# Performance work log

Measured on AMD Instinct MI355X. Metric: run time of the kernel, lower is better.

## Reference

```python
import jax, jax.numpy as jnp
import numpy as np

V_FEATS = 1024; N1 = 800; N2 = 800; K = 10
CONV = [256, 128]; DENSE = [256, 64]


def setup_inputs() -> dict:
    key = jax.random.key(0)
    ks = jax.random.split(key, 20)
    inp = {
        "Z1": jax.random.normal(ks[0], (N1, V_FEATS), jnp.float32),
        "nb1": jax.random.randint(ks[2], (N1, K), -1, N1),
        "Z2": jax.random.normal(ks[1], (N2, V_FEATS), jnp.float32),
        "nb2": jax.random.randint(ks[3], (N2, K), -1, N2),
    }
    j = 4
    dims = [V_FEATS] + CONV
    for i, (di, do) in enumerate(zip(dims[:-1], dims[1:])):
        s = 1.0 / np.sqrt(di)
        inp[f"Wr{i}"] = jax.random.normal(ks[j], (di, do), jnp.float32) * s; j += 1
        inp[f"Wnr{i}"] = jax.random.normal(ks[j], (di, do), jnp.float32) * s; j += 1
    fdims = [2 * CONV[-1]] + DENSE + [1]
    for i, (di, do) in enumerate(zip(fdims[:-1], fdims[1:])):
        s = 1.0 / np.sqrt(di)
        inp[f"fW{i}"] = jax.random.normal(ks[j], (di, do), jnp.float32) * s; j += 1
        inp[f"fb{i}"] = jnp.zeros((do,), jnp.float32)
    return inp


def gnn_layer(Z, nb, Wr, Wnr):
    # residue (self) signal and neighbor base signal
    res = Z @ Wr                                  # [N, F]
    base = Z @ Wnr                                # [N, F]
    mask = nb > -1                                # [N, K]
    feats = base[nb] * mask[..., None]            # gather (neg idx wrap, masked out)
    norm = jnp.maximum(mask.sum(1), 1).astype(Z.dtype)  # [N], avoid div-by-0
    return jax.nn.relu(res + feats.sum(1) / norm[:, None])


def _forward(Z1, nb1, Z2, nb2, Wr0, Wnr0, Wr1, Wnr1, fW0, fb0, fW1, fb1, fW2, fb2):
    # two stacked GNN layers per protein (shared weights across the two proteins)
    x1 = gnn_layer(gnn_layer(Z1, nb1, Wr0, Wnr0), nb1, Wr1, Wnr1)  # [N1, F]
    x2 = gnn_layer(gnn_layer(Z2, nb2, Wr0, Wnr0), nb2, Wr1, Wnr1)  # [N2, F]
    n1, F = x1.shape
    n2 = x2.shape[0]
    # all-pairs concat: itertools.product(rows(x1), rows(x2)) -> [N1*N2, 2F]
    pairs = jnp.concatenate(
        [jnp.broadcast_to(x1[:, None, :], (n1, n2, F)),
         jnp.broadcast_to(x2[None, :, :], (n1, n2, F))], axis=-1
    ).reshape(n1 * n2, 2 * F)
    h = jax.nn.relu(pairs @ fW0 + fb0)
    h = jax.nn.relu(h @ fW1 + fb1)
    return jnp.squeeze(h @ fW2 + fb2)             # [N1*N2]


def reference(Z1, nb1, Z2, nb2, Wr0, Wnr0, Wr1, Wnr1, fW0, fb0, fW1, fb1, fW2, fb2):
    return _forward(Z1, nb1, Z2, nb2, Wr0, Wnr0, Wr1, Wnr1,
                    fW0, fb0, fW1, fb1, fW2, fb2)
```

## Files before the change

kernel.cpp:

```cpp
#include <hip/hip_runtime.h>
#include <hip/hip_bf16.h>
#include <cstdint>
#include <cstddef>


typedef __bf16 bf16_t;
typedef __bf16 bf16x4 __attribute__((ext_vector_type(4)));
typedef __bf16 bf16x8 __attribute__((ext_vector_type(8)));
typedef float f32x4 __attribute__((ext_vector_type(4)));
typedef _Float16 f16_t;
typedef _Float16 f16x8 __attribute__((ext_vector_type(8)));

static __device__ __forceinline__ f32x4 mfma_bf16(bf16x8 a, bf16x8 b, f32x4 c) {
  return __builtin_amdgcn_mfma_f32_16x16x32_bf16(a, b, c, 0, 0, 0);
}
static __device__ __forceinline__ f32x4 mfma_f16(f16x8 a, f16x8 b, f32x4 c) {
  return __builtin_amdgcn_mfma_f32_16x16x32_f16(a, b, c, 0, 0, 0);
}

#define N1R 800
#define NR  1600
#define VF  1024
#define F0  256
#define F1  128

static __device__ __forceinline__ void split8(float4 va, float4 vb,
                                              bf16x8& h8, bf16x8& l8) {
  float v[8] = {va.x, va.y, va.z, va.w, vb.x, vb.y, vb.z, vb.w};
  #pragma unroll
  for (int e = 0; e < 8; ++e) {
    bf16_t h = (bf16_t)v[e];
    h8[e] = h;
    l8[e] = (bf16_t)(v[e] - (float)h);
  }
}

__global__ void conv_agg(const float* __restrict__ Z1, const float* __restrict__ Z2,
                         const int* __restrict__ nb1, const int* __restrict__ nb2,
                         const float* __restrict__ Wr0, const float* __restrict__ Wnr0,
                         const float* __restrict__ Wr1, const float* __restrict__ Wnr1,
                         const float* __restrict__ fW0, const float* __restrict__ fW1,
                         const float* __restrict__ fb1, const float* __restrict__ fW2,
                         const float* __restrict__ fb2,
                         bf16_t* __restrict__ W0h, bf16_t* __restrict__ W0l,
                         bf16_t* __restrict__ W1h, bf16_t* __restrict__ W1l,
                         bf16_t* __restrict__ fAh, bf16_t* __restrict__ fAl,
                         bf16_t* __restrict__ fBh, bf16_t* __restrict__ fBl,
                         f16_t* __restrict__ fW1th, float* __restrict__ fbw,
                         bf16_t* __restrict__ Zah, bf16_t* __restrict__ Zal) {
  int wb = blockIdx.x;
  int tid = threadIdx.x;
  if (wb >= 2625) {
    int r = wb - 2625;
    const int* nbp;
    const float* Zp;
    if (r < N1R) { nbp = nb1 + r * 10; Zp = Z1; }
    else         { nbp = nb2 + (r - N1R) * 10; Zp = Z2; }
    int c4 = tid * 4;
    float4 s = make_float4(0.f, 0.f, 0.f, 0.f);
    int cnt = 0;
    #pragma unroll
    for (int k = 0; k < 10; ++k) {
      int idx = nbp[k];
      if (idx > -1) {
        cnt++;
        float4 v = *(const float4*)(Zp + (size_t)idx * VF + c4);
        s.x += v.x; s.y += v.y; s.z += v.z; s.w += v.w;
      }
    }
    float inv = 1.f / (float)(cnt > 0 ? cnt : 1);
    float vv[4] = {s.x * inv, s.y * inv, s.z * inv, s.w * inv};
    bf16x4 h4, l4;
    #pragma unroll
    for (int e = 0; e < 4; ++e) {
      bf16_t h = (bf16_t)vv[e];
      h4[e] = h;
      l4[e] = (bf16_t)(vv[e] - (float)h);
    }
    *(bf16x4*)(Zah + (size_t)r * VF + c4) = h4;
    *(bf16x4*)(Zal + (size_t)r * VF + c4) = l4;
    return;
  }
  if (wb >= 2560 && wb < 2624) {
    int t = (wb - 2560) * 256 + tid;
    int n = t & 63;
    int k = t >> 6;
    fW1th[(n << 8) + k] = (f16_t)fW1[k * 64 + n];
    return;
  }
  if (wb == 2624) {
    if (tid < 128) {
      int jl = tid & 15, s = tid >> 4;
      fbw[jl * 8 + s] = (s < 4) ? fb1[s * 16 + jl] : fW2[(s - 4) * 16 + jl];
    } else if (tid == 128) {
      fbw[128] = fb2[0];
    }
    return;
  }
  const float* src; bf16_t* dh; bf16_t* dl; int ld, lk, ln, b0;
  if      (wb < 1024) { src = Wr0;  ld = 256; lk = 10; ln = 8; dh = W0h;              dl = W0l;              b0 = 0;    }
  else if (wb < 2048) { src = Wnr0; ld = 256; lk = 10; ln = 8; dh = W0h + 256 * 1024; dl = W0l + 256 * 1024; b0 = 1024; }
  else if (wb < 2176) { src = Wr1;  ld = 128; lk = 8;  ln = 7; dh = W1h;              dl = W1l;              b0 = 2048; }
  else if (wb < 2304) { src = Wnr1; ld = 128; lk = 8;  ln = 7; dh = W1h + 128 * 256;  dl = W1l + 128 * 256;  b0 = 2176; }
  else if (wb < 2432) { src = fW0;             ld = 256; lk = 7; ln = 8; dh = fAh;    dl = fAl;              b0 = 2304; }
  else                { src = fW0 + 128 * 256; ld = 256; lk = 7; ln = 8; dh = fBh;    dl = fBl;              b0 = 2432; }
  int t = (wb - b0) * 256 + tid;
  int n = t & ((1 << ln) - 1);
  int k = t >> ln;
  float v = src[k * ld + n];
  bf16_t h = (bf16_t)v;
  dh[(n << lk) + k] = h;
  dl[(n << lk) + k] = (bf16_t)(v - (float)h);
}

__global__ __launch_bounds__(256) void gemm_l1(
    const float* __restrict__ Z1, const float* __restrict__ Z2,
    const bf16_t* __restrict__ Zah, const bf16_t* __restrict__ Zal,
    const bf16_t* __restrict__ W0h, const bf16_t* __restrict__ W0l,
    float* __restrict__ P) {
  int lane = threadIdx.x & 63;
  int w = threadIdx.x >> 6;
  int jl = lane & 15, hi = lane >> 4;

  int row0 = blockIdx.y * 16;
  int col = blockIdx.x * 64 + w * 16 + jl;
  int z = blockIdx.z;
  int half = z >> 1;
  int kStart = (z & 1) * 512;
  int r = row0 + jl;

  const size_t WOFF = (size_t)half * 256 * 1024;
  const bf16_t* pBh = W0h + WOFF + (size_t)col * 1024 + hi * 8 + kStart;
  const bf16_t* pBl = W0l + WOFF + (size_t)col * 1024 + hi * 8 + kStart;

  f32x4 accE = {}, accO = {};
  if (half == 0) {
    const float* pZ = ((r < N1R) ? Z1 + (size_t)r * VF
                                 : Z2 + (size_t)(r - N1R) * VF) + hi * 8 + kStart;
    for (int kb = 0; kb < 512; kb += 128) {
      float4 za[4][2];
      bf16x8 bh[4], bl[4];
      #pragma unroll
      for (int u = 0; u < 4; ++u) {
        za[u][0] = *(const float4*)(pZ + kb + u * 32);
        za[u][1] = *(const float4*)(pZ + kb + u * 32 + 4);
        bh[u] = *(const bf16x8*)(pBh + kb + u * 32);
        bl[u] = *(const bf16x8*)(pBl + kb + u * 32);
      }
      #pragma unroll
      for (int u = 0; u < 4; ++u) {
        bf16x8 ah, al;
        split8(za[u][0], za[u][1], ah, al);
        f32x4& acc = (u & 1) ? accO : accE;
        acc = mfma_bf16(ah, bh[u], acc);
        acc = mfma_bf16(al, bh[u], acc);
        acc = mfma_bf16(ah, bl[u], acc);
      }
    }
  } else {
    const bf16_t* pAh = Zah + (size_t)r * VF + hi * 8 + kStart;
    const bf16_t* pAl = Zal + (size_t)r * VF + hi * 8 + kStart;
    for (int kb = 0; kb < 512; kb += 128) {
      bf16x8 ah[4], al[4], bh[4], bl[4];
      #pragma unroll
      for (int u = 0; u < 4; ++u) {
        ah[u] = *(const bf16x8*)(pAh + kb + u * 32);
        al[u] = *(const bf16x8*)(pAl + kb + u * 32);
        bh[u] = *(const bf16x8*)(pBh + kb + u * 32);
        bl[u] = *(const bf16x8*)(pBl + kb + u * 32);
      }
      #pragma unroll
      for (int u = 0; u < 4; ++u) {
        f32x4& acc = (u & 1) ? accO : accE;
        acc = mfma_bf16(ah[u], bh[u], acc);
        acc = mfma_bf16(al[u], bh[u], acc);
        acc = mfma_bf16(ah[u], bl[u], acc);
      }
    }
  }
  float* Pz = P + (size_t)z * NR * F0;
  #pragma unroll
  for (int reg = 0; reg < 4; ++reg) {
    int row = row0 + hi * 4 + reg;
    Pz[(size_t)row * F0 + col] = accE[reg] + accO[reg];
  }
}

__global__ void agg1_kernel(const float* __restrict__ P,
                            const int* __restrict__ nb1, const int* __restrict__ nb2,
                            bf16_t* __restrict__ H0h, bf16_t* __restrict__ H0l,
                            bf16_t* __restrict__ Gah, bf16_t* __restrict__ Gal) {
  int r = blockIdx.x;
  int c = threadIdx.x;
  const size_t PS = (size_t)NR * F0;
  const int* nbp;
  int roff;
  if (r < N1R) { nbp = nb1 + r * 10; roff = 0; }
  else         { nbp = nb2 + (r - N1R) * 10; roff = N1R; }
  size_t so = (size_t)r * F0 + c;
  float v = fmaxf(P[so] + P[so + PS] + P[so + 2 * PS] + P[so + 3 * PS], 0.f);
  bf16_t h = (bf16_t)v;
  H0h[so] = h;
  H0l[so] = (bf16_t)(v - (float)h);
  float s = 0.f; int cnt = 0;
  #pragma unroll
  for (int k = 0; k < 10; ++k) {
    int idx = nbp[k];
    if (idx > -1) {
      cnt++;
      size_t o = (size_t)(roff + idx) * F0 + c;
      s += fmaxf(P[o] + P[o + PS] + P[o + 2 * PS] + P[o + 3 * PS], 0.f);
    }
  }
  float g = s / (float)(cnt > 0 ? cnt : 1);
  bf16_t gh = (bf16_t)g;
  Gah[so] = gh;
  Gal[so] = (bf16_t)(g - (float)gh);
}

__global__ __launch_bounds__(256) void gemm_l2(
    const bf16_t* __restrict__ H0h, const bf16_t* __restrict__ H0l,
    const bf16_t* __restrict__ Gah, const bf16_t* __restrict__ Gal,
    const bf16_t* __restrict__ W1h, const bf16_t* __restrict__ W1l,
    float* __restrict__ P2) {
  int lane = threadIdx.x & 63;
  int w = threadIdx.x >> 6;
  int jl = lane & 15, hi = lane >> 4;

  int row0 = blockIdx.y * 16;
  int col = blockIdx.x * 64 + w * 16 + jl;
  int z = blockIdx.z;
  int r = row0 + jl;

  const bf16_t* pAh = (z ? Gah : H0h) + (size_t)r * F0 + hi * 8;
  const bf16_t* pAl = (z ? Gal : H0l) + (size_t)r * F0 + hi * 8;
  const size_t WOFF = (size_t)z * 128 * 256;
  const bf16_t* pBh = W1h + WOFF + (size_t)col * 256 + hi * 8;
  const bf16_t* pBl = W1l + WOFF + (size_t)col * 256 + hi * 8;

  f32x4 accE = {}, accO = {};
  for (int kb = 0; kb < 256; kb += 128) {
    bf16x8 ah[4], al[4], bh[4], bl[4];
    #pragma unroll
    for (int u = 0; u < 4; ++u) {
      ah[u] = *(const bf16x8*)(pAh + kb + u * 32);
      al[u] = *(const bf16x8*)(pAl + kb + u * 32);
      bh[u] = *(const bf16x8*)(pBh + kb + u * 32);
      bl[u] = *(const bf16x8*)(pBl + kb + u * 32);
    }
    #pragma unroll
    for (int u = 0; u < 4; ++u) {
      f32x4& acc = (u & 1) ? accO : accE;
      acc = mfma_bf16(ah[u], bh[u], acc);
      acc = mfma_bf16(al[u], bh[u], acc);
      acc = mfma_bf16(ah[u], bl[u], acc);
    }
  }
  float* Pz = P2 + (size_t)z * NR * F1;
  #pragma unroll
  for (int reg = 0; reg < 4; ++reg) {
    int row = row0 + hi * 4 + reg;
    Pz[(size_t)row * F1 + col] = accE[reg] + accO[reg];
  }
}

__global__ __launch_bounds__(256) void gemm_dual(
    const float* __restrict__ P2,
    const bf16_t* __restrict__ fAh, const bf16_t* __restrict__ fAl,
    const bf16_t* __restrict__ fBh, const bf16_t* __restrict__ fBl,
    const float* __restrict__ fb0, f16_t* __restrict__ ABh) {
  int lane = threadIdx.x & 63;
  int w = threadIdx.x >> 6;
  int jl = lane & 15, hi = lane >> 4;

  int row0 = blockIdx.y * 16;
  int col = blockIdx.x * 64 + w * 16 + jl;
  int r = row0 + jl;
  bool isA = (row0 < N1R);

  const float* pP0 = P2 + (size_t)r * F1 + hi * 8;
  const float* pP1 = pP0 + (size_t)NR * F1;
  const bf16_t* pBh = (isA ? fAh : fBh) + (size_t)col * F1 + hi * 8;
  const bf16_t* pBl = (isA ? fAl : fBl) + (size_t)col * F1 + hi * 8;

  float4 p0[4][2], p1[4][2];
  bf16x8 bh[4], bl[4];
  #pragma unroll
  for (int u = 0; u < 4; ++u) {
    p0[u][0] = *(const float4*)(pP0 + u * 32);
    p0[u][1] = *(const float4*)(pP0 + u * 32 + 4);
    p1[u][0] = *(const float4*)(pP1 + u * 32);
    p1[u][1] = *(const float4*)(pP1 + u * 32 + 4);
    bh[u] = *(const bf16x8*)(pBh + u * 32);
    bl[u] = *(const bf16x8*)(pBl + u * 32);
  }
  f32x4 accE = {}, accO = {};
  #pragma unroll
  for (int u = 0; u < 4; ++u) {
    float4 s0 = make_float4(fmaxf(p0[u][0].x + p1[u][0].x, 0.f),
                            fmaxf(p0[u][0].y + p1[u][0].y, 0.f),
                            fmaxf(p0[u][0].z + p1[u][0].z, 0.f),
                            fmaxf(p0[u][0].w + p1[u][0].w, 0.f));
    float4 s1 = make_float4(fmaxf(p0[u][1].x + p1[u][1].x, 0.f),
                            fmaxf(p0[u][1].y + p1[u][1].y, 0.f),
                            fmaxf(p0[u][1].z + p1[u][1].z, 0.f),
                            fmaxf(p0[u][1].w + p1[u][1].w, 0.f));
    bf16x8 ah, al;
    split8(s0, s1, ah, al);
    f32x4& acc = (u & 1) ? accO : accE;
    acc = mfma_bf16(ah, bh[u], acc);
    acc = mfma_bf16(al, bh[u], acc);
    acc = mfma_bf16(ah, bl[u], acc);
  }

  float bv = isA ? fb0[col] : 0.f;
  #pragma unroll
  for (int reg = 0; reg < 4; ++reg) {
    int row = row0 + hi * 4 + reg;
    ABh[(size_t)row * 256 + col] = (f16_t)(accE[reg] + accO[reg] + bv);
  }
}

#define IBLK 2
#define ITILE 16
__global__ __launch_bounds__(256) void pair_kernel(
    const f16_t* __restrict__ ABh, const f16_t* __restrict__ W1th,
    const float* __restrict__ fbw, float* __restrict__ out) {
  __shared__ alignas(16) unsigned char sWh[64 * 512];
  __shared__ alignas(16) f16_t sA[ITILE * 256];

  const int tid = threadIdx.x;
  const int lane = tid & 63;
  const int w = tid >> 6;
  const int jl = lane & 15;
  const int hi = lane >> 4;
  const int j0 = blockIdx.x * 64;
  const int i0 = blockIdx.y * ITILE;

  #pragma unroll
  for (int s = 0; s < 8; ++s) {
    int c = tid + 256 * s;
    int n = c >> 5;
    int cb = (c & 31) << 4;
    int sw = cb ^ ((n & 7) << 4);
    *(uint4*)(sWh + n * 512 + sw) = *(const uint4*)((const unsigned char*)W1th + n * 512 + cb);
  }
  #pragma unroll
  for (int s = 0; s < 2; ++s) {
    int c = tid + 256 * s;
    int rr = c >> 5;
    int cc = c & 31;
    *(uint4*)((unsigned char*)sA + rr * 512 + cc * 16) =
        *(const uint4*)(ABh + (size_t)(i0 + rr) * 256 + cc * 8);
  }

  int j = j0 + w * 16 + jl;
  f16x8 breg[8];
  {
    const f16_t* Bp = ABh + (size_t)(N1R + j) * 256;
    bool ok = (j < N1R);
    f16x8 z{};
    #pragma unroll
    for (int t = 0; t < 8; ++t)
      breg[t] = ok ? *(const f16x8*)(Bp + t * 32 + hi * 8) : z;
  }

  float4 fb1r = *(const float4*)(fbw + jl * 8);
  float4 fw2r = *(const float4*)(fbw + jl * 8 + 4);
  float bias2 = fbw[128];

  __syncthreads();

  #pragma unroll 1
  for (int ig = 0; ig < ITILE / IBLK; ++ig) {
    f32x4 acc[IBLK][4] = {};
    #pragma unroll
    for (int t = 0; t < 8; ++t) {
      f16x8 bv = breg[t];
      f16x8 af[IBLK];
      const f16x8 Zv{};
      #pragma unroll
      for (int ib = 0; ib < IBLK; ++ib) {
        f16x8 av = *(const f16x8*)(sA + (ig * IBLK + ib) * 256 + t * 32 + hi * 8);
        af[ib] = __builtin_elementwise_max(av + bv, Zv);
      }
      int kbyte = t * 64 + hi * 16;
      #pragma unroll
      for (int nf = 0; nf < 4; ++nf) {
        int n = nf * 16 + jl;
        f16x8 wh = *(const f16x8*)(sWh + n * 512 + (kbyte ^ ((n & 7) << 4)));
        #pragma unroll
        for (int ib = 0; ib < IBLK; ++ib)
          acc[ib][nf] = mfma_f16(af[ib], wh, acc[ib][nf]);
      }
    }
    float fb1a[4] = {fb1r.x, fb1r.y, fb1r.z, fb1r.w};
    float fw2a[4] = {fw2r.x, fw2r.y, fw2r.z, fw2r.w};
    #pragma unroll
    for (int ib = 0; ib < IBLK; ++ib) {
      float part[4];
      #pragma unroll
      for (int r = 0; r < 4; ++r) {
        float ssum = 0.f;
        #pragma unroll
        for (int nf = 0; nf < 4; ++nf) {
          float h = acc[ib][nf][r] + fb1a[nf];
          h = fmaxf(h, 0.f);
          ssum += h * fw2a[nf];
        }
        part[r] = ssum;
      }
      #pragma unroll
      for (int off = 1; off < 16; off <<= 1) {
        #pragma unroll
        for (int r = 0; r < 4; ++r) part[r] += __shfl_xor(part[r], off, 64);
      }
      if (jl == 0) {
        int jo = j0 + w * 16 + hi * 4;
        if (jo < N1R) {
          float4 o = make_float4(part[0] + bias2, part[1] + bias2,
                                 part[2] + bias2, part[3] + bias2);
          *(float4*)(out + (size_t)(i0 + ig * IBLK + ib) * 800 + jo) = o;
        }
      }
    }
  }
}

extern "C" void kernel_launch(void* const* d_in, const int* in_sizes, int n_in,
                              void* d_out, int out_size, void* d_ws, size_t ws_size,
                              hipStream_t stream) {
  const float* Z1   = (const float*)d_in[0];
  const int*   nb1  = (const int*)d_in[1];
  const float* Z2   = (const float*)d_in[2];
  const int*   nb2  = (const int*)d_in[3];
  const float* Wr0  = (const float*)d_in[4];
  const float* Wnr0 = (const float*)d_in[5];
  const float* Wr1  = (const float*)d_in[6];
  const float* Wnr1 = (const float*)d_in[7];
  const float* fW0  = (const float*)d_in[8];
  const float* fb0  = (const float*)d_in[9];
  const float* fW1  = (const float*)d_in[10];
  const float* fb1  = (const float*)d_in[11];
  const float* fW2  = (const float*)d_in[12];
  const float* fb2  = (const float*)d_in[13];
  float* out = (float*)d_out;

  char* p = (char*)d_ws;
  auto alloc = [&](size_t bytes) {
    char* q = p;
    p += (bytes + 255) & ~(size_t)255;
    return q;
  };
  bf16_t* W0h   = (bf16_t*)alloc((size_t)512 * 1024 * 2);
  bf16_t* W0l   = (bf16_t*)alloc((size_t)512 * 1024 * 2);
  bf16_t* W1h   = (bf16_t*)alloc((size_t)256 * 256 * 2);
  bf16_t* W1l   = (bf16_t*)alloc((size_t)256 * 256 * 2);
  bf16_t* fAh   = (bf16_t*)alloc((size_t)256 * 128 * 2);
  bf16_t* fAl   = (bf16_t*)alloc((size_t)256 * 128 * 2);
  bf16_t* fBh   = (bf16_t*)alloc((size_t)256 * 128 * 2);
  bf16_t* fBl   = (bf16_t*)alloc((size_t)256 * 128 * 2);
  f16_t*  fW1th = (f16_t*)alloc((size_t)64 * 256 * 2);
  float*  fbw   = (float*)alloc(129 * 4);
  bf16_t* Zah   = (bf16_t*)alloc((size_t)NR * VF * 2);
  bf16_t* Zal   = (bf16_t*)alloc((size_t)NR * VF * 2);
  float*  P01   = (float*)alloc((size_t)4 * NR * F0 * 4);
  bf16_t* H0h   = (bf16_t*)alloc((size_t)NR * F0 * 2);
  bf16_t* H0l   = (bf16_t*)alloc((size_t)NR * F0 * 2);
  bf16_t* Gah   = (bf16_t*)alloc((size_t)NR * F0 * 2);
  bf16_t* Gal   = (bf16_t*)alloc((size_t)NR * F0 * 2);
  float*  P2    = (float*)alloc((size_t)2 * NR * F1 * 4);
  f16_t*  ABh   = (f16_t*)alloc((size_t)NR * 256 * 2);
  (void)in_sizes; (void)n_in; (void)out_size; (void)ws_size;

  conv_agg<<<4225, 256, 0, stream>>>(Z1, Z2, nb1, nb2, Wr0, Wnr0, Wr1, Wnr1,
                                     fW0, fW1, fb1, fW2, fb2,
                                     W0h, W0l, W1h, W1l, fAh, fAl, fBh, fBl,
                                     fW1th, fbw, Zah, Zal);
  gemm_l1<<<dim3(4, 100, 4), 256, 0, stream>>>(Z1, Z2, Zah, Zal, W0h, W0l, P01);
  agg1_kernel<<<NR, 256, 0, stream>>>(P01, nb1, nb2, H0h, H0l, Gah, Gal);
  gemm_l2<<<dim3(2, 100, 2), 256, 0, stream>>>(H0h, H0l, Gah, Gal, W1h, W1l, P2);
  gemm_dual<<<dim3(4, 100), 256, 0, stream>>>(P2, fAh, fAl, fBh, fBl, fb0, ABh);
  pair_kernel<<<dim3(13, 50), 256, 0, stream>>>(ABh, fW1th, fbw, out);
}
```

Baseline: 125.3 us.

## Widen gemm_l1 block tile to all columns and double-buffer operand loads

Each wave now computes four 16x16 column fragments (64 columns), so one block covers all 256 output columns of a 16-row tile. Each A fragment (including the fp32-to-bf16 split) is loaded and converted once and reused across four MFMA column groups instead of being refetched by four separate blocks. The k-loop becomes a two-stage software pipeline that prefetches the next 32-wide slice while the current one is consumed. The grid shrinks from 1600 to 400 blocks, which raises register pressure and may cut occupancy and parallelism on a large GPU.

```diff
diff --git a/kernel.cpp b/kernel.cpp
--- a/kernel.cpp
+++ b/kernel.cpp
@@ -113,6 +113,23 @@
   dl[(n << lk) + k] = (bf16_t)(v - (float)h);
 }
 
+#define CONSUME_F32(ZA, ZB, BH, BL)                      \
+  { bf16x8 ah_, al_; split8(ZA, ZB, ah_, al_);           \
+    _Pragma("unroll")                                    \
+    for (int cf = 0; cf < 4; ++cf) {                     \
+      acc[cf] = mfma_bf16(ah_, BH[cf], acc[cf]);         \
+      acc[cf] = mfma_bf16(al_, BH[cf], acc[cf]);         \
+      acc[cf] = mfma_bf16(ah_, BL[cf], acc[cf]);         \
+    } }
+
+#define CONSUME_BF16(AH, AL, BH, BL)                     \
+  { _Pragma("unroll")                                    \
+    for (int cf = 0; cf < 4; ++cf) {                     \
+      acc[cf] = mfma_bf16(AH, BH[cf], acc[cf]);          \
+      acc[cf] = mfma_bf16(AL, BH[cf], acc[cf]);          \
+      acc[cf] = mfma_bf16(AH, BL[cf], acc[cf]);          \
+    } }
+
 __global__ __launch_bounds__(256) void gemm_l1(
     const float* __restrict__ Z1, const float* __restrict__ Z2,
     const bf16_t* __restrict__ Zah, const bf16_t* __restrict__ Zal,
@@ -122,67 +139,117 @@
   int w = threadIdx.x >> 6;
   int jl = lane & 15, hi = lane >> 4;
 
-  int row0 = blockIdx.y * 16;
-  int col = blockIdx.x * 64 + w * 16 + jl;
-  int z = blockIdx.z;
+  int row0 = blockIdx.x * 16;
+  int z = blockIdx.y;
   int half = z >> 1;
   int kStart = (z & 1) * 512;
   int r = row0 + jl;
 
   const size_t WOFF = (size_t)half * 256 * 1024;
-  const bf16_t* pBh = W0h + WOFF + (size_t)col * 1024 + hi * 8 + kStart;
-  const bf16_t* pBl = W0l + WOFF + (size_t)col * 1024 + hi * 8 + kStart;
-
-  f32x4 accE = {}, accO = {};
+  const bf16_t* pBh[4];
+  const bf16_t* pBl[4];
+  #pragma unroll
+  for (int cf = 0; cf < 4; ++cf) {
+    int col = w * 64 + cf * 16 + jl;
+    pBh[cf] = W0h + WOFF + (size_t)col * 1024 + hi * 8 + kStart;
+    pBl[cf] = W0l + WOFF + (size_t)col * 1024 + hi * 8 + kStart;
+  }
+
+  f32x4 acc[4] = {};
+
   if (half == 0) {
     const float* pZ = ((r < N1R) ? Z1 + (size_t)r * VF
                                  : Z2 + (size_t)(r - N1R) * VF) + hi * 8 + kStart;
-    for (int kb = 0; kb < 512; kb += 128) {
-      float4 za[4][2];
-      bf16x8 bh[4], bl[4];
-      #pragma unroll
-      for (int u = 0; u < 4; ++u) {
-        za[u][0] = *(const float4*)(pZ + kb + u * 32);
-        za[u][1] = *(const float4*)(pZ + kb + u * 32 + 4);
-        bh[u] = *(const bf16x8*)(pBh + kb + u * 32);
-        bl[u] = *(const bf16x8*)(pBl + kb + u * 32);
-      }
-      #pragma unroll
-      for (int u = 0; u < 4; ++u) {
-        bf16x8 ah, al;
-        split8(za[u][0], za[u][1], ah, al);
-        f32x4& acc = (u & 1) ? accO : accE;
-        acc = mfma_bf16(ah, bh[u], acc);
-        acc = mfma_bf16(al, bh[u], acc);
-        acc = mfma_bf16(ah, bl[u], acc);
-      }
-    }
+    float4 za0, zb0, za1, zb1;
+    bf16x8 bh0[4], bl0[4], bh1[4], bl1[4];
+    za0 = *(const float4*)(pZ + 0);
+    zb0 = *(const float4*)(pZ + 4);
+    #pragma unroll
+    for (int cf = 0; cf < 4; ++cf) {
+      bh0[cf] = *(const bf16x8*)(pBh[cf] + 0);
+      bl0[cf] = *(const bf16x8*)(pBl[cf] + 0);
+    }
+    za1 = *(const float4*)(pZ + 32);
+    zb1 = *(const float4*)(pZ + 36);
+    #pragma unroll
+    for (int cf = 0; cf < 4; ++cf) {
+      bh1[cf] = *(const bf16x8*)(pBh[cf] + 32);
+      bl1[cf] = *(const bf16x8*)(pBl[cf] + 32);
+    }
+    #pragma unroll 1
+    for (int it = 0; it < 7; ++it) {
+      int kb = it * 64;
+      CONSUME_F32(za0, zb0, bh0, bl0)
+      za0 = *(const float4*)(pZ + kb + 64);
+      zb0 = *(const float4*)(pZ + kb + 68);
+      #pragma unroll
+      for (int cf = 0; cf < 4; ++cf) {
+        bh0[cf] = *(const bf16x8*)(pBh[cf] + kb + 64);
+        bl0[cf] = *(const bf16x8*)(pBl[cf] + kb + 64);
+      }
+      CONSUME_F32(za1, zb1, bh1, bl1)
+      za1 = *(const float4*)(pZ + kb + 96);
+      zb1 = *(const float4*)(pZ + kb + 100);
+      #pragma unroll
+      for (int cf = 0; cf < 4; ++cf) {
+        bh1[cf] = *(const bf16x8*)(pBh[cf] + kb + 96);
+        bl1[cf] = *(const bf16x8*)(pBl[cf] + kb + 96);
+      }
+    }
+    CONSUME_F32(za0, zb0, bh0, bl0)
+    CONSUME_F32(za1, zb1, bh1, bl1)
   } else {
     const bf16_t* pAh = Zah + (size_t)r * VF + hi * 8 + kStart;
     const bf16_t* pAl = Zal + (size_t)r * VF + hi * 8 + kStart;
-    for (int kb = 0; kb < 512; kb += 128) {
-      bf16x8 ah[4], al[4], bh[4], bl[4];
-      #pragma unroll
-      for (int u = 0; u < 4; ++u) {
-        ah[u] = *(const bf16x8*)(pAh + kb + u * 32);
-        al[u] = *(const bf16x8*)(pAl + kb + u * 32);
-        bh[u] = *(const bf16x8*)(pBh + kb + u * 32);
-        bl[u] = *(const bf16x8*)(pBl + kb + u * 32);
-      }
-      #pragma unroll
-      for (int u = 0; u < 4; ++u) {
-        f32x4& acc = (u & 1) ? accO : accE;
-        acc = mfma_bf16(ah[u], bh[u], acc);
-        acc = mfma_bf16(al[u], bh[u], acc);
-        acc = mfma_bf16(ah[u], bl[u], acc);
-      }
-    }
-  }
+    bf16x8 ah0, al0, ah1, al1;
+    bf16x8 bh0[4], bl0[4], bh1[4], bl1[4];
+    ah0 = *(const bf16x8*)(pAh + 0);
+    al0 = *(const bf16x8*)(pAl + 0);
+    #pragma unroll
+    for (int cf = 0; cf < 4; ++cf) {
+      bh0[cf] = *(const bf16x8*)(pBh[cf] + 0);
+      bl0[cf] = *(const bf16x8*)(pBl[cf] + 0);
+    }
+    ah1 = *(const bf16x8*)(pAh + 32);
+    al1 = *(const bf16x8*)(pAl + 32);
+    #pragma unroll
+    for (int cf = 0; cf < 4; ++cf) {
+      bh1[cf] = *(const bf16x8*)(pBh[cf] + 32);
+      bl1[cf] = *(const bf16x8*)(pBl[cf] + 32);
+    }
+    #pragma unroll 1
+    for (int it = 0; it < 7; ++it) {
+      int kb = it * 64;
+      CONSUME_BF16(ah0, al0, bh0, bl0)
+      ah0 = *(const bf16x8*)(pAh + kb + 64);
+      al0 = *(const bf16x8*)(pAl + kb + 64);
+      #pragma unroll
+      for (int cf = 0; cf < 4; ++cf) {
+        bh0[cf] = *(const bf16x8*)(pBh[cf] + kb + 64);
+        bl0[cf] = *(const bf16x8*)(pBl[cf] + kb + 64);
+      }
+      CONSUME_BF16(ah1, al1, bh1, bl1)
+      ah1 = *(const bf16x8*)(pAh + kb + 96);
+      al1 = *(const bf16x8*)(pAl + kb + 96);
+      #pragma unroll
+      for (int cf = 0; cf < 4; ++cf) {
+        bh1[cf] = *(const bf16x8*)(pBh[cf] + kb + 96);
+        bl1[cf] = *(const bf16x8*)(pBl[cf] + kb + 96);
+      }
+    }
+    CONSUME_BF16(ah0, al0, bh0, bl0)
+    CONSUME_BF16(ah1, al1, bh1, bl1)
+  }
+
   float* Pz = P + (size_t)z * NR * F0;
   #pragma unroll
-  for (int reg = 0; reg < 4; ++reg) {
-    int row = row0 + hi * 4 + reg;
-    Pz[(size_t)row * F0 + col] = accE[reg] + accO[reg];
+  for (int cf = 0; cf < 4; ++cf) {
+    int col = w * 64 + cf * 16 + jl;
+    #pragma unroll
+    for (int reg = 0; reg < 4; ++reg) {
+      int row = row0 + hi * 4 + reg;
+      Pz[(size_t)row * F0 + col] = acc[cf][reg];
+    }
   }
 }
 
@@ -477,7 +544,7 @@
                                      fW0, fW1, fb1, fW2, fb2,
                                      W0h, W0l, W1h, W1l, fAh, fAl, fBh, fBl,
                                      fW1th, fbw, Zah, Zal);
-  gemm_l1<<<dim3(4, 100, 4), 256, 0, stream>>>(Z1, Z2, Zah, Zal, W0h, W0l, P01);
+  gemm_l1<<<dim3(100, 4), 256, 0, stream>>>(Z1, Z2, Zah, Zal, W0h, W0l, P01);
   agg1_kernel<<<NR, 256, 0, stream>>>(P01, nb1, nb2, H0h, H0l, Gah, Gal);
   gemm_l2<<<dim3(2, 100, 2), 256, 0, stream>>>(H0h, H0l, Gah, Gal, W1h, W1l, P2);
   gemm_dual<<<dim3(4, 100), 256, 0, stream>>>(P2, fAh, fAl, fBh, fBl, fb0, ABh);
```

Measured after the change: 112.0 us, median of 2. -10.7%, faster.
